# Kernel optimization log

Hardware: AMD Instinct MI355X
Metric: run time of the kernel (lower is better)

## Reference

```python
import jax, jax.numpy as jnp
import numpy as np

NC = 100000   # output rows of the sparse matrix
NT = 100000   # input columns of the sparse matrix
NNZ = 640000  # number of nonzeros (COO entries)
D = 128       # dense feature width


def setup_inputs() -> dict:
    key = jax.random.key(0)
    k1, k2, k3 = jax.random.split(key, 3)
    mat = jax.random.normal(k1, (NT, D), dtype=jnp.float32)
    row = jax.random.randint(k2, (NNZ,), 0, NC, dtype=jnp.int32)
    col = jax.random.randint(k3, (NNZ,), 0, NT, dtype=jnp.int32)
    return {"mat": mat, "row": row, "col": col}


def reference(mat, row, col):
    # Sparse binary (Nc x Nt) @ dense (Nt x D):
    # out[r] += mat[c] for each nonzero (r, c).
    # The TF original batches gather + tensor_scatter_nd_add over the
    # index list; a single gather + segment_sum computes the same result.
    vals = jnp.take(mat, col, axis=0)                      # [nnz, D]
    out = jax.ops.segment_sum(vals, row, num_segments=NC)  # [Nc, D]
    return out
```

## Files before the change

kernel.cpp:

```cpp
#include <hip/hip_runtime.h>


#define NC_CONST 100000
#define NNZ_CONST 640000
#define D_CONST 128
#define NXCD 8
#define RANGE 12500
#define NBINS 1536
#define RPB 66
#define G1 128
#define EPB (NNZ_CONST / G1)
#define E4 1024
#define BINCAP 640
#define OVF2_MAX 4096
#define K3_BLOCKS 2048
#define K4_BLOCKS ((NC_CONST + RPB - 1) / RPB)
#define COLMASK 0x1FFFFu
#define CSPLIT 1048576

typedef float v4f __attribute__((ext_vector_type(4)));
typedef unsigned short u16;
typedef u16 v4u16 __attribute__((ext_vector_type(4)));

__device__ __forceinline__ float bf16_to_f32(u16 b) {
    return __uint_as_float((unsigned)b << 16);
}

__device__ __forceinline__ v4u16 cvt_bf16x4(v4f v) {
    v4u16 o;
    #pragma unroll
    for (int k = 0; k < 4; ++k) {
        unsigned u = __float_as_uint(v[k]);
        o[k] = (u16)((u + 0x7FFFu + ((u >> 16) & 1u)) >> 16);
    }
    return o;
}

__global__ __launch_bounds__(256) void hist_convert_kernel(
    const int* __restrict__ row, const float* __restrict__ mat,
    int* __restrict__ hist_g, int* __restrict__ ovf_cnt,
    u16* __restrict__ matb) {
    const int t = threadIdx.x;
    const int b = blockIdx.x;

    if (b >= G1) {
        const int cb = b - G1;
        const int stride = (K3_BLOCKS - G1) * 256;
        const v4f* mat4 = reinterpret_cast<const v4f*>(mat);
        v4u16* matb4 = reinterpret_cast<v4u16*>(matb);
        #pragma unroll 1
        for (int i = cb * 256 + t; i < CSPLIT; i += stride) {
            const v4f v = __builtin_nontemporal_load(mat4 + i);
            matb4[i] = cvt_bf16x4(v);
        }
        return;
    }

    __shared__ int h[NBINS];
    if (b == 0 && t == 0) *ovf_cnt = 0;
    for (int i = t; i < NBINS; i += 256) h[i] = 0;
    __syncthreads();
    const int4* row4 = reinterpret_cast<const int4*>(row + b * EPB);
    for (int i = t; i < EPB / 4; i += 256) {
        int4 r4 = row4[i];
        atomicAdd(&h[r4.x / RPB], 1);
        atomicAdd(&h[r4.y / RPB], 1);
        atomicAdd(&h[r4.z / RPB], 1);
        atomicAdd(&h[r4.w / RPB], 1);
    }
    __syncthreads();
    for (int i = t; i < NBINS; i += 256)
        hist_g[(size_t)i * G1 + b] = h[i];
}

__global__ __launch_bounds__(128) void scan_bins_kernel(
    int* __restrict__ hist_g, int* __restrict__ binSum) {
    __shared__ int v[G1];
    const int bin = blockIdx.x;
    const int t = threadIdx.x;
    const int orig = hist_g[(size_t)bin * G1 + t];
    v[t] = orig;
    __syncthreads();
    #pragma unroll
    for (int off = 1; off < G1; off <<= 1) {
        int add = (t >= off) ? v[t - off] : 0;
        __syncthreads();
        v[t] += add;
        __syncthreads();
    }
    if (t == G1 - 1) binSum[bin] = v[t];
    hist_g[(size_t)bin * G1 + t] = v[t] - orig;
}

__global__ __launch_bounds__(256) void sort_convert_kernel(
    const int* __restrict__ row, const int* __restrict__ col,
    const float* __restrict__ mat,
    const int* __restrict__ hist_g,
    unsigned* __restrict__ sorted_g, u16* __restrict__ matb,
    int* __restrict__ ovf_cnt, int* __restrict__ ovf) {
    __shared__ int runStart[NBINS];
    __shared__ int cur[NBINS];
    __shared__ int lbase[NBINS];
    __shared__ int part[256];
    __shared__ unsigned sv[EPB];
    __shared__ u16 sbin[EPB];
    const int t = threadIdx.x;
    const int b = blockIdx.x;

    if (b >= G1) {
        const int cb = b - G1;
        const int total4 = NC_CONST * D_CONST / 4;
        const int stride = (K3_BLOCKS - G1) * 256;
        const v4f* mat4 = reinterpret_cast<const v4f*>(mat);
        v4u16* matb4 = reinterpret_cast<v4u16*>(matb);
        #pragma unroll 1
        for (int i = CSPLIT + cb * 256 + t; i < total4; i += stride) {
            const v4f v = __builtin_nontemporal_load(mat4 + i);
            matb4[i] = cvt_bf16x4(v);
        }
        return;
    }

    for (int i = t; i < NBINS; i += 256) {
        runStart[i] = 0;
        lbase[i] = hist_g[(size_t)i * G1 + b];
    }
    __syncthreads();
    const int4* row4 = reinterpret_cast<const int4*>(row + b * EPB);
    const int4* col4 = reinterpret_cast<const int4*>(col + b * EPB);
    for (int i = t; i < EPB / 4; i += 256) {
        int4 r4 = row4[i];
        atomicAdd(&runStart[r4.x / RPB], 1);
        atomicAdd(&runStart[r4.y / RPB], 1);
        atomicAdd(&runStart[r4.z / RPB], 1);
        atomicAdd(&runStart[r4.w / RPB], 1);
    }
    __syncthreads();
    int loc[6];
    int acc = 0;
    #pragma unroll
    for (int k = 0; k < 6; ++k) { acc += runStart[t * 6 + k]; loc[k] = acc; }
    part[t] = acc;
    const int tot = acc;
    __syncthreads();
    #pragma unroll
    for (int off = 1; off < 256; off <<= 1) {
        int add = (t >= off) ? part[t - off] : 0;
        __syncthreads();
        part[t] += add;
        __syncthreads();
    }
    const int prefix = part[t] - tot;
    #pragma unroll
    for (int k = 0; k < 6; ++k) {
        int idx = t * 6 + k;
        runStart[idx] = prefix + loc[k] - runStart[idx];
    }
    __syncthreads();
    for (int i = t; i < NBINS; i += 256) cur[i] = runStart[i];
    __syncthreads();
    for (int i = t; i < EPB / 4; i += 256) {
        int4 r4 = row4[i];
        int4 c4 = col4[i];
        #pragma unroll
        for (int k = 0; k < 4; ++k) {
            int r = (&r4.x)[k];
            int c = (&c4.x)[k];
            int bin = r / RPB;
            int rl = r - bin * RPB;
            int s = atomicAdd(&cur[bin], 1);
            sv[s] = ((unsigned)rl << 17) | (unsigned)c;
            sbin[s] = (u16)bin;
        }
    }
    __syncthreads();
    for (int s = t; s < EPB; s += 256) {
        int bin = sbin[s];
        int within = lbase[bin] + (s - runStart[bin]);
        if (within < BINCAP) {
            sorted_g[(size_t)bin * BINCAP + within] = sv[s];
        } else {
            int o = atomicAdd(ovf_cnt, 1);
            if (o < OVF2_MAX) {
                unsigned v = sv[s];
                ovf[2 * o] = bin * RPB + (int)(v >> 17);
                ovf[2 * o + 1] = (int)(v & COLMASK);
            }
        }
    }
}

__global__ __launch_bounds__(256) void bin_segsum_kernel(
    const u16* __restrict__ matb, const unsigned* __restrict__ sorted_g,
    const int* __restrict__ binSum,
    const int* __restrict__ ovf_cnt, const int* __restrict__ ovf,
    float* __restrict__ out) {
    __shared__ int bufA[E4];
    __shared__ int cols[E4];
    __shared__ int h[128];
    __shared__ int cur[RPB];
    const int t = threadIdx.x;
    const int bin = blockIdx.x;
    const int r0 = bin * RPB;
    const int start = bin * BINCAP;
    int cnt = binSum[bin];
    if (cnt > BINCAP) cnt = BINCAP;
    const int grp = t >> 5;
    const int lane = t & 31;
    const int novf = *ovf_cnt;

    int n = cnt;

    for (int i = t; i < 128; i += 256) h[i] = 0;
    __syncthreads();
    for (int i = t; i < n; i += 256) {
        unsigned v = sorted_g[start + i];
        bufA[i] = (int)v;
        atomicAdd(&h[v >> 17], 1);
    }
    __syncthreads();
    #pragma unroll
    for (int off = 1; off < 128; off <<= 1) {
        int add = 0;
        if (t < 128 && t >= off) add = h[t - off];
        __syncthreads();
        if (t < 128) h[t] += add;
        __syncthreads();
    }
    for (int i = t; i < RPB; i += 256) cur[i] = (i == 0) ? 0 : h[i - 1];
    __syncthreads();
    for (int i = t; i < n; i += 256) {
        unsigned v = (unsigned)bufA[i];
        int s = atomicAdd(&cur[v >> 17], 1);
        cols[s] = (int)(v & COLMASK);
    }
    __syncthreads();

    for (int rl = grp; rl < RPB; rl += 8) {
        int r = r0 + rl;
        if (r >= NC_CONST) break;
        int s0 = (rl == 0) ? 0 : h[rl - 1];
        int nr = h[rl] - s0;
        float ax = 0.f, ay = 0.f, az = 0.f, aw = 0.f;
        const int nm1 = nr - 1;
        for (int j = 0; j < nr; j += 4) {
            int c0 = cols[s0 + j];
            int c1 = cols[s0 + min(j + 1, nm1)];
            int c2 = cols[s0 + min(j + 2, nm1)];
            int c3 = cols[s0 + min(j + 3, nm1)];
            const v4u16 b0 = reinterpret_cast<const v4u16*>(matb + (size_t)c0 * D_CONST)[lane];
            const v4u16 b1 = reinterpret_cast<const v4u16*>(matb + (size_t)c1 * D_CONST)[lane];
            const v4u16 b2 = reinterpret_cast<const v4u16*>(matb + (size_t)c2 * D_CONST)[lane];
            const v4u16 b3 = reinterpret_cast<const v4u16*>(matb + (size_t)c3 * D_CONST)[lane];
            float s1 = (j + 1 < nr) ? 1.f : 0.f;
            float s2 = (j + 2 < nr) ? 1.f : 0.f;
            float s3 = (j + 3 < nr) ? 1.f : 0.f;
            ax += bf16_to_f32(b0[0]) + s1 * bf16_to_f32(b1[0]) + s2 * bf16_to_f32(b2[0]) + s3 * bf16_to_f32(b3[0]);
            ay += bf16_to_f32(b0[1]) + s1 * bf16_to_f32(b1[1]) + s2 * bf16_to_f32(b2[1]) + s3 * bf16_to_f32(b3[1]);
            az += bf16_to_f32(b0[2]) + s1 * bf16_to_f32(b1[2]) + s2 * bf16_to_f32(b2[2]) + s3 * bf16_to_f32(b3[2]);
            aw += bf16_to_f32(b0[3]) + s1 * bf16_to_f32(b1[3]) + s2 * bf16_to_f32(b2[3]) + s3 * bf16_to_f32(b3[3]);
        }
        for (int o = 0; o < novf && o < OVF2_MAX; ++o) {
            if (ovf[2 * o] == r) {
                int c = ovf[2 * o + 1];
                const v4u16 b = reinterpret_cast<const v4u16*>(matb + (size_t)c * D_CONST)[lane];
                ax += bf16_to_f32(b[0]);
                ay += bf16_to_f32(b[1]);
                az += bf16_to_f32(b[2]);
                aw += bf16_to_f32(b[3]);
            }
        }
        v4f rr;
        rr.x = ax; rr.y = ay; rr.z = az; rr.w = aw;
        __builtin_nontemporal_store(
            rr, reinterpret_cast<v4f*>(out + (size_t)r * D_CONST) + lane);
    }
}

#define OVF_MAX 65536
template <int CAP>
__global__ __launch_bounds__(256) void place_xcd_kernel(
    const int* __restrict__ row, const int* __restrict__ col,
    int* __restrict__ cnt, int* __restrict__ ovf_cnt,
    int* __restrict__ ovf, int* __restrict__ bucket) {
    const int xcd = blockIdx.x % NXCD;
    const int gidx = blockIdx.x / NXCD;
    const int lo = xcd * RANGE;
    const int hi = lo + RANGE;
    const int nthreads = (2048 / NXCD) * 256;
    const int4* row4 = reinterpret_cast<const int4*>(row);
    const int4* col4 = reinterpret_cast<const int4*>(col);
    const int n4 = NNZ_CONST / 4;
    for (int i = gidx * 256 + threadIdx.x; i < n4; i += nthreads) {
        int4 r4 = row4[i];
        int4 c4 = col4[i];
        #pragma unroll
        for (int k = 0; k < 4; ++k) {
            int r = (&r4.x)[k];
            if (r >= lo && r < hi) {
                int c = (&c4.x)[k];
                int idx = atomicAdd(&cnt[r], 1);
                if (idx < CAP) bucket[(size_t)r * CAP + idx] = c;
                else { int o = atomicAdd(ovf_cnt, 1);
                       if (o < OVF_MAX) { ovf[2 * o] = r; ovf[2 * o + 1] = c; } }
            }
        }
    }
}

template <int CAP>
__global__ __launch_bounds__(256) void segsum_xcd_kernel(
    const float* __restrict__ mat, const int* __restrict__ cnt,
    const int* __restrict__ ovf_cnt, const int* __restrict__ ovf,
    const int* __restrict__ bucket, float* __restrict__ out) {
    const int xcd = blockIdx.x % NXCD;
    const int local = blockIdx.x / NXCD;
    int g = xcd * RANGE + local * 8 + (threadIdx.x >> 5);
    int lane = threadIdx.x & 31;
    if (g >= xcd * RANGE + RANGE) return;
    int n = cnt[g];
    if (n > CAP) n = CAP;
    int myc = (lane < n) ? bucket[(size_t)g * CAP + lane] : 0;
    float ax = 0.f, ay = 0.f, az = 0.f, aw = 0.f;
    for (int j = 0; j < n; ++j) {
        int c = __shfl(myc, j, 32);
        const float4 v = reinterpret_cast<const float4*>(mat + (size_t)c * D_CONST)[lane];
        ax += v.x; ay += v.y; az += v.z; aw += v.w;
    }
    int novf = *ovf_cnt;
    if (novf > OVF_MAX) novf = OVF_MAX;
    for (int o = 0; o < novf; ++o) {
        if (ovf[2 * o] == g) {
            int c = ovf[2 * o + 1];
            const float4 v = reinterpret_cast<const float4*>(mat + (size_t)c * D_CONST)[lane];
            ax += v.x; ay += v.y; az += v.z; aw += v.w;
        }
    }
    v4f r; r.x = ax; r.y = ay; r.z = az; r.w = aw;
    __builtin_nontemporal_store(r, reinterpret_cast<v4f*>(out + (size_t)g * D_CONST) + lane);
}

__global__ __launch_bounds__(256) void scatter_add_kernel(
    const float* __restrict__ mat, const int* __restrict__ row,
    const int* __restrict__ col, float* __restrict__ out) {
    int gid = blockIdx.x * blockDim.x + threadIdx.x;
    int nz = gid >> 5;
    int lane = gid & 31;
    if (nz >= NNZ_CONST) return;
    int r = row[nz];
    int c = col[nz];
    const float4 v = reinterpret_cast<const float4*>(mat + (size_t)c * D_CONST)[lane];
    float* o = out + (size_t)r * D_CONST + (size_t)lane * 4;
    atomicAdd(o + 0, v.x);
    atomicAdd(o + 1, v.y);
    atomicAdd(o + 2, v.z);
    atomicAdd(o + 3, v.w);
}

extern "C" void kernel_launch(void* const* d_in, const int* in_sizes, int n_in,
                              void* d_out, int out_size, void* d_ws, size_t ws_size,
                              hipStream_t stream) {
    const float* mat = (const float*)d_in[0];
    const int* row   = (const int*)d_in[1];
    const int* col   = (const int*)d_in[2];
    float* out = (float*)d_out;

    const size_t matb_elems = (size_t)NC_CONST * D_CONST;
    const size_t ints_main = (size_t)NBINS * G1 + NBINS + 1 + 2 * OVF2_MAX
                             + (size_t)NBINS * BINCAP;
    const size_t need_main = matb_elems * sizeof(u16) + ints_main * sizeof(int);

    constexpr int CAP = 32;
    const size_t ints_t2 =
        (size_t)NC_CONST + 1 + 2 * OVF_MAX + (size_t)NC_CONST * CAP;
    const size_t need_t2 = ints_t2 * sizeof(int);

    if (ws_size >= need_main) {
        u16* matb        = (u16*)d_ws;
        int* hist        = (int*)(matb + matb_elems);
        int* binSum      = hist + (size_t)NBINS * G1;
        int* ovf_cnt     = binSum + NBINS;
        int* ovf         = ovf_cnt + 1;
        unsigned* sorted = (unsigned*)(ovf + 2 * OVF2_MAX);

        hist_convert_kernel<<<K3_BLOCKS, 256, 0, stream>>>(
            row, mat, hist, ovf_cnt, matb);
        scan_bins_kernel<<<NBINS, 128, 0, stream>>>(hist, binSum);
        sort_convert_kernel<<<K3_BLOCKS, 256, 0, stream>>>(
            row, col, mat, hist, sorted, matb, ovf_cnt, ovf);
        bin_segsum_kernel<<<K4_BLOCKS, 256, 0, stream>>>(
            matb, sorted, binSum, ovf_cnt, ovf, out);
    } else if (ws_size >= need_t2) {
        int* cnt     = (int*)d_ws;
        int* ovf_cnt = cnt + NC_CONST;
        int* ovf     = ovf_cnt + 1;
        int* bucket  = ovf + 2 * OVF_MAX;
        (void)hipMemsetAsync(cnt, 0, (size_t)(NC_CONST + 1) * sizeof(int), stream);
        place_xcd_kernel<CAP><<<2048, 256, 0, stream>>>(
            row, col, cnt, ovf_cnt, ovf, bucket);
        segsum_xcd_kernel<CAP><<<(((RANGE + 7) / 8) * NXCD), 256, 0, stream>>>(
            mat, cnt, ovf_cnt, ovf, bucket, out);
    } else {
        (void)hipMemsetAsync(out, 0, (size_t)out_size * sizeof(float), stream);
        const long long total = (long long)NNZ_CONST * 32;
        scatter_add_kernel<<<(int)((total + 255) / 256), 256, 0, stream>>>(
            mat, row, col, out);
    }
}
```

Measured before the change: 151.5 us.

## Fold bin scan into sort kernel and reuse stored per-block histograms

Removes the separate scan_bins kernel launch. Each sorting block now computes its exclusive bin offsets by summing the histograms of all preceding blocks, stored block-major so reads are coalesced. It also drops the recount of its own rows in favour of reading its stored histogram, and the last block writes the bin totals. In exchange, later blocks do up to 127 serial passes over 1536 ints, an O(G1^2) redundant read load that may lengthen the critical path.

```diff
diff --git a/kernel.cpp b/kernel.cpp
--- a/kernel.cpp
+++ b/kernel.cpp
@@ -70,32 +70,13 @@
     }
     __syncthreads();
     for (int i = t; i < NBINS; i += 256)
-        hist_g[(size_t)i * G1 + b] = h[i];
-}
-
-__global__ __launch_bounds__(128) void scan_bins_kernel(
-    int* __restrict__ hist_g, int* __restrict__ binSum) {
-    __shared__ int v[G1];
-    const int bin = blockIdx.x;
-    const int t = threadIdx.x;
-    const int orig = hist_g[(size_t)bin * G1 + t];
-    v[t] = orig;
-    __syncthreads();
-    #pragma unroll
-    for (int off = 1; off < G1; off <<= 1) {
-        int add = (t >= off) ? v[t - off] : 0;
-        __syncthreads();
-        v[t] += add;
-        __syncthreads();
-    }
-    if (t == G1 - 1) binSum[bin] = v[t];
-    hist_g[(size_t)bin * G1 + t] = v[t] - orig;
+        hist_g[(size_t)b * NBINS + i] = h[i];
 }
 
 __global__ __launch_bounds__(256) void sort_convert_kernel(
     const int* __restrict__ row, const int* __restrict__ col,
     const float* __restrict__ mat,
-    const int* __restrict__ hist_g,
+    const int* __restrict__ hist_g, int* __restrict__ binSum,
     unsigned* __restrict__ sorted_g, u16* __restrict__ matb,
     int* __restrict__ ovf_cnt, int* __restrict__ ovf) {
     __shared__ int runStart[NBINS];
@@ -121,21 +102,37 @@
         return;
     }
 
-    for (int i = t; i < NBINS; i += 256) {
-        runStart[i] = 0;
-        lbase[i] = hist_g[(size_t)i * G1 + b];
-    }
-    __syncthreads();
-    const int4* row4 = reinterpret_cast<const int4*>(row + b * EPB);
-    const int4* col4 = reinterpret_cast<const int4*>(col + b * EPB);
-    for (int i = t; i < EPB / 4; i += 256) {
-        int4 r4 = row4[i];
-        atomicAdd(&runStart[r4.x / RPB], 1);
-        atomicAdd(&runStart[r4.y / RPB], 1);
-        atomicAdd(&runStart[r4.z / RPB], 1);
-        atomicAdd(&runStart[r4.w / RPB], 1);
-    }
-    __syncthreads();
+    {
+        int acc0 = 0, acc1 = 0, acc2 = 0, acc3 = 0, acc4 = 0, acc5 = 0;
+        #pragma unroll 1
+        for (int bp = 0; bp < b; ++bp) {
+            const int* hrow = hist_g + (size_t)bp * NBINS;
+            acc0 += hrow[t];
+            acc1 += hrow[t + 256];
+            acc2 += hrow[t + 512];
+            acc3 += hrow[t + 768];
+            acc4 += hrow[t + 1024];
+            acc5 += hrow[t + 1280];
+        }
+        lbase[t]        = acc0;
+        lbase[t + 256]  = acc1;
+        lbase[t + 512]  = acc2;
+        lbase[t + 768]  = acc3;
+        lbase[t + 1024] = acc4;
+        lbase[t + 1280] = acc5;
+        const int* hown = hist_g + (size_t)b * NBINS;
+        runStart[t]        = hown[t];
+        runStart[t + 256]  = hown[t + 256];
+        runStart[t + 512]  = hown[t + 512];
+        runStart[t + 768]  = hown[t + 768];
+        runStart[t + 1024] = hown[t + 1024];
+        runStart[t + 1280] = hown[t + 1280];
+    }
+    __syncthreads();
+    if (b == G1 - 1) {
+        for (int i = t; i < NBINS; i += 256)
+            binSum[i] = lbase[i] + runStart[i];
+    }
     int loc[6];
     int acc = 0;
     #pragma unroll
@@ -159,6 +156,8 @@
     __syncthreads();
     for (int i = t; i < NBINS; i += 256) cur[i] = runStart[i];
     __syncthreads();
+    const int4* row4 = reinterpret_cast<const int4*>(row + b * EPB);
+    const int4* col4 = reinterpret_cast<const int4*>(col + b * EPB);
     for (int i = t; i < EPB / 4; i += 256) {
         int4 r4 = row4[i];
         int4 c4 = col4[i];
@@ -366,7 +365,7 @@
     float* out = (float*)d_out;
 
     const size_t matb_elems = (size_t)NC_CONST * D_CONST;
-    const size_t ints_main = (size_t)NBINS * G1 + NBINS + 1 + 2 * OVF2_MAX
+    const size_t ints_main = (size_t)G1 * NBINS + NBINS + 1 + 2 * OVF2_MAX
                              + (size_t)NBINS * BINCAP;
     const size_t need_main = matb_elems * sizeof(u16) + ints_main * sizeof(int);
 
@@ -378,16 +377,15 @@
     if (ws_size >= need_main) {
         u16* matb        = (u16*)d_ws;
         int* hist        = (int*)(matb + matb_elems);
-        int* binSum      = hist + (size_t)NBINS * G1;
+        int* binSum      = hist + (size_t)G1 * NBINS;
         int* ovf_cnt     = binSum + NBINS;
         int* ovf         = ovf_cnt + 1;
         unsigned* sorted = (unsigned*)(ovf + 2 * OVF2_MAX);
 
         hist_convert_kernel<<<K3_BLOCKS, 256, 0, stream>>>(
             row, mat, hist, ovf_cnt, matb);
-        scan_bins_kernel<<<NBINS, 128, 0, stream>>>(hist, binSum);
         sort_convert_kernel<<<K3_BLOCKS, 256, 0, stream>>>(
-            row, col, mat, hist, sorted, matb, ovf_cnt, ovf);
+            row, col, mat, hist, binSum, sorted, matb, ovf_cnt, ovf);
         bin_segsum_kernel<<<K4_BLOCKS, 256, 0, stream>>>(
             matb, sorted, binSum, ovf_cnt, ovf, out);
     } else if (ws_size >= need_t2) {
```

Result: slower. 162.2 us (+7.1%).
